# Performance work log

Hardware: AMD Instinct MI355X
Metric: run time of the kernel (lower is better)

Reference implementation:

```python
import jax, jax.numpy as jnp
import numpy as np

L, D, S, K, V, R, E, C = 256, 300, 16, 16, 100000, 6, 2048, 7
SW = 1            # slide_win; window = 2*SW+1 = 3
LAMB = 0.5
NEG = -1e9


def setup_inputs() -> dict:
    key = jax.random.key(0)
    ks = jax.random.split(key, 24)
    utt_emb = jax.random.normal(ks[0], (L, D), jnp.float32)
    str_src = jax.random.randint(ks[1], (E,), 0, L)
    str_dst = jax.random.randint(ks[2], (E,), 0, L)
    str_edge_type = jax.random.randint(ks[3], (E,), 0, R)
    src_ids = jax.random.randint(ks[4], (3, L, S), 0, V)
    src_valid = jax.random.uniform(ks[5], (3, L, S)) < 0.9
    cpt_src_ids = jnp.where(src_valid, src_ids, -1)
    dst_ids = jax.random.randint(ks[6], (3, L, S, K), 0, V)
    dst_valid = jnp.logical_and(jax.random.uniform(ks[7], (3, L, S, K)) < 0.8, src_valid[..., None])
    cpt_dst_ids = jnp.where(dst_valid, dst_ids, -1)
    cpt_weight = jax.random.uniform(ks[8], (3, L, S, K), jnp.float32)
    cpt_sentic = jax.random.normal(ks[9], (3, L, S, K), jnp.float32) * 0.5
    cpt_table = jax.random.normal(ks[10], (V, D), jnp.float32) * 0.02
    W_basis = jax.random.normal(ks[11], (2, D, D), jnp.float32) * 0.02
    comp = jax.random.normal(ks[12], (R, 2), jnp.float32)
    W_self = jax.random.normal(ks[13], (D, D), jnp.float32) * 0.02
    b_rgcn = jnp.zeros((D,), jnp.float32)
    Wq = jax.random.normal(ks[14], (D, D), jnp.float32) * 0.02
    Wk = jax.random.normal(ks[15], (D, D), jnp.float32) * 0.02
    Wv = jax.random.normal(ks[16], (D, D), jnp.float32) * 0.02
    Wo = jax.random.normal(ks[17], (D, D), jnp.float32) * 0.02
    r_vecs = jax.random.uniform(ks[18], (3, D), jnp.float32)  # isa/causes/hcontext relation vectors
    W_fuse = jax.random.normal(ks[19], (3 * D, D), jnp.float32) * 0.02
    b_fuse = jnp.zeros((D,), jnp.float32)
    W_out = jax.random.normal(ks[20], (D, C), jnp.float32) * 0.02
    b_out = jnp.zeros((C,), jnp.float32)
    return dict(utt_emb=utt_emb, str_src=str_src, str_dst=str_dst, str_edge_type=str_edge_type,
                cpt_src_ids=cpt_src_ids, cpt_dst_ids=cpt_dst_ids, cpt_weight=cpt_weight,
                cpt_sentic=cpt_sentic, cpt_table=cpt_table, W_basis=W_basis, comp=comp,
                W_self=W_self, b_rgcn=b_rgcn, Wq=Wq, Wk=Wk, Wv=Wv, Wo=Wo, r_vecs=r_vecs,
                W_fuse=W_fuse, b_fuse=b_fuse, W_out=W_out, b_out=b_out)


def reference(utt_emb, str_src, str_dst, str_edge_type, cpt_src_ids, cpt_dst_ids,
              cpt_weight, cpt_sentic, cpt_table, W_basis, comp, W_self, b_rgcn,
              Wq, Wk, Wv, Wo, r_vecs, W_fuse, b_fuse, W_out, b_out):
    H, dh, W = 2, D // 2, 2 * SW + 1
    # ---- RelGraphConv (basis decomposition, num_bases=2, sum aggregation + self-loop) ----
    W_rel = jnp.einsum('rb,bio->rio', comp, W_basis)                       # [R,D,D]
    msg = jnp.einsum('ei,eio->eo', utt_emb[str_src], W_rel[str_edge_type])  # [E,D]
    hidden_rgcn = jax.ops.segment_sum(msg, str_dst, num_segments=L) + utt_emb @ W_self + b_rgcn
    # ---- RelAtt: multi-head attention over sliding window, keep center utterance ----
    ids = jnp.concatenate([jnp.zeros((SW,), jnp.int32), jnp.arange(L, dtype=jnp.int32), jnp.full((SW,), L - 1, jnp.int32)])
    win = ids[jnp.arange(L)[:, None] + jnp.arange(W)[None, :]]             # [L,W]
    x = utt_emb[win]                                                       # [L,W,D]
    sh = lambda t: t.reshape(L, W, H, dh).transpose(0, 2, 1, 3)
    q, k, v = sh(x @ Wq), sh(x @ Wk), sh(x @ Wv)
    attn = jax.nn.softmax(jnp.einsum('lhqd,lhkd->lhqk', q, k) / jnp.sqrt(jnp.float32(dh)), axis=-1)
    relatt_out = (jnp.einsum('lhqk,lhkd->lhqd', attn, v).transpose(0, 2, 1, 3).reshape(L, W, D) @ Wo)[:, SW, :]
    # ---- symbolic reasoning over 3 relation types (padded, vectorized) ----
    src_mask = cpt_src_ids >= 0                                            # [3,L,S]
    dst_mask = cpt_dst_ids >= 0                                            # [3,L,S,K]
    src_emb = cpt_table[jnp.maximum(cpt_src_ids, 0)]                       # [3,L,S,D]
    dst_emb = cpt_table[jnp.maximum(cpt_dst_ids, 0)]                       # [3,L,S,K,D]
    u = relatt_out[None, :, None, None, :]                                 # [1,L,1,1,D]
    cos = jnp.abs(jnp.sum(u * dst_emb, -1) / (jnp.linalg.norm(relatt_out, axis=-1)[None, :, None, None] * jnp.linalg.norm(dst_emb, axis=-1) + 1e-8))
    omega = LAMB * cpt_weight * cos + (1.0 - LAMB) * jnp.abs(cpt_sentic)
    alpha1 = jax.nn.softmax(jnp.where(dst_mask, omega, NEG), axis=-1) * dst_mask  # [3,L,S,K]
    cpt = alpha1[..., None] * dst_emb                                      # [3,L,S,K,D]
    re_dot = r_vecs[:, None, None, None, :] * cpt                          # relation-weighted neighbor emb
    s = jnp.sum(src_emb[..., None, :] * re_dot, -1)                        # [3,L,S,K]
    alpha2 = jax.nn.softmax(jnp.where(dst_mask, s, NEG), axis=-1) * dst_mask
    src2 = src_emb + jnp.sum(alpha2[..., None] * re_dot, axis=3)           # [3,L,S,D]
    nodes = src2.transpose(1, 0, 2, 3).reshape(L, 3 * S, D)
    node_mask = src_mask.transpose(1, 0, 2).reshape(L, 3 * S)
    score = jnp.einsum('lnd,ld->ln', nodes, relatt_out)
    att = jax.nn.softmax(jnp.where(node_mask, score, NEG), axis=-1) * node_mask
    sym = jnp.einsum('ln,lnd->ld', att, nodes)
    sym = sym * jnp.any(node_mask, axis=-1, keepdims=True)                 # symbolic_mask
    # ---- fusion + classifier ----
    feat = jnp.concatenate([hidden_rgcn, relatt_out, sym], axis=-1)        # [L,3D]
    return jax.nn.log_softmax(jax.nn.relu(feat @ W_fuse + b_fuse) @ W_out + b_out, axis=-1)
```

## Files before the change

kernel.cpp:

```cpp
#include <hip/hip_runtime.h>
#include <math.h>

#define Lq 256
#define Dm 300
#define Sq 16
#define Kc 16
#define Eq 2048
#define D4 75

__global__ __launch_bounds__(256) void mm6_kernel(
    const float* __restrict__ utt,
    const float* __restrict__ Wb,
    const float* __restrict__ Wself,
    const float* __restrict__ brgcn,
    const float* __restrict__ Wq,
    const float* __restrict__ Wk,
    const float* __restrict__ Wv,
    float* __restrict__ P0, float* __restrict__ P1,
    float* __restrict__ Hrg, float* __restrict__ Q,
    float* __restrict__ Km, float* __restrict__ Vm)
{
    const int m = blockIdx.y;
    const float* W; float* Y; const float* bias = nullptr;
    switch (m) {
      case 0: W = Wb;          Y = P0; break;
      case 1: W = Wb + 90000;  Y = P1; break;
      case 2: W = Wself;       Y = Hrg; bias = brgcn; break;
      case 3: W = Wq;          Y = Q; break;
      case 4: W = Wk;          Y = Km; break;
      default: W = Wv;         Y = Vm; break;
    }
    const int row0 = blockIdx.x * 4;
    __shared__ float xs[4][Dm];
    for (int i = threadIdx.x; i < 4*Dm; i += 256)
        xs[i/Dm][i%Dm] = utt[(row0 + i/Dm)*Dm + (i%Dm)];
    __syncthreads();
    for (int c = threadIdx.x; c < Dm; c += 256) {
        float a0=0.f,a1=0.f,a2=0.f,a3=0.f;
        #pragma unroll 10
        for (int d = 0; d < Dm; ++d) {
            float wv = W[d*Dm + c];
            a0 += xs[0][d]*wv; a1 += xs[1][d]*wv;
            a2 += xs[2][d]*wv; a3 += xs[3][d]*wv;
        }
        float b = bias ? bias[c] : 0.f;
        Y[(row0+0)*Dm+c] = a0+b;
        Y[(row0+1)*Dm+c] = a1+b;
        Y[(row0+2)*Dm+c] = a2+b;
        Y[(row0+3)*Dm+c] = a3+b;
    }
}

__global__ __launch_bounds__(256) void mm4row_kernel(
    const float* __restrict__ X, const float* __restrict__ W, float* __restrict__ Y)
{
    const int row0 = blockIdx.x * 4;
    __shared__ float xs[4][Dm];
    for (int i = threadIdx.x; i < 4*Dm; i += 256)
        xs[i/Dm][i%Dm] = X[(row0 + i/Dm)*Dm + (i%Dm)];
    __syncthreads();
    for (int c = threadIdx.x; c < Dm; c += 256) {
        float a0=0.f,a1=0.f,a2=0.f,a3=0.f;
        #pragma unroll 10
        for (int d = 0; d < Dm; ++d) {
            float wv = W[d*Dm + c];
            a0 += xs[0][d]*wv; a1 += xs[1][d]*wv;
            a2 += xs[2][d]*wv; a3 += xs[3][d]*wv;
        }
        Y[(row0+0)*Dm+c] = a0;
        Y[(row0+1)*Dm+c] = a1;
        Y[(row0+2)*Dm+c] = a2;
        Y[(row0+3)*Dm+c] = a3;
    }
}

__global__ __launch_bounds__(64) void rgcn_edge_kernel(
    const int* __restrict__ src, const int* __restrict__ dst, const int* __restrict__ et,
    const float* __restrict__ comp, const float* __restrict__ P0,
    const float* __restrict__ P1, float* __restrict__ Hrg)
{
    int e = blockIdx.x;
    int s = src[e], d = dst[e], r = et[e];
    float c0 = comp[r*2], c1 = comp[r*2+1];
    for (int i = threadIdx.x; i < Dm; i += 64) {
        float msg = c0*P0[s*Dm+i] + c1*P1[s*Dm+i];
        atomicAdd(&Hrg[d*Dm+i], msg);
    }
}

__global__ __launch_bounds__(64) void winattn_kernel(
    const float* __restrict__ Q, const float* __restrict__ Kmat,
    const float* __restrict__ Vmat, float* __restrict__ ctx)
{
    int l = blockIdx.x;
    int lane = threadIdx.x;
    int w0 = l > 0 ? l-1 : 0;
    int w1 = l;
    int w2 = l < Lq-1 ? l+1 : Lq-1;
    int win[3] = {w0, w1, w2};
    __shared__ float sc[2][3];
    for (int h = 0; h < 2; ++h) {
      for (int w = 0; w < 3; ++w) {
        float acc = 0.f;
        const float* qp = Q + l*Dm + h*150;
        const float* kp = Kmat + win[w]*Dm + h*150;
        for (int d = lane; d < 150; d += 64) acc += qp[d]*kp[d];
        for (int off = 32; off > 0; off >>= 1) acc += __shfl_down(acc, off);
        if (lane == 0) sc[h][w] = acc * 0.081649658092772603f;
      }
    }
    __syncthreads();
    float attn[2][3];
    for (int h = 0; h < 2; ++h) {
      float m = fmaxf(sc[h][0], fmaxf(sc[h][1], sc[h][2]));
      float e0 = expf(sc[h][0]-m), e1 = expf(sc[h][1]-m), e2 = expf(sc[h][2]-m);
      float iz = 1.f/(e0+e1+e2);
      attn[h][0]=e0*iz; attn[h][1]=e1*iz; attn[h][2]=e2*iz;
    }
    for (int d = lane; d < Dm; d += 64) {
      int h = d / 150;
      ctx[l*Dm+d] = attn[h][0]*Vmat[w0*Dm+d] + attn[h][1]*Vmat[w1*Dm+d]
                  + attn[h][2]*Vmat[w2*Dm+d];
    }
}

__global__ __launch_bounds__(64) void rownorm_kernel(
    const float* __restrict__ X, float* __restrict__ nrm)
{
    int l = blockIdx.x;
    float acc = 0.f;
    for (int d = threadIdx.x; d < Dm; d += 64) { float v = X[l*Dm+d]; acc += v*v; }
    for (int off = 32; off > 0; off >>= 1) acc += __shfl_down(acc, off);
    if (threadIdx.x == 0) nrm[l] = sqrtf(acc);
}

__global__ __launch_bounds__(256) void concept_kernel(
    const int* __restrict__ src_ids,
    const int* __restrict__ dst_ids,
    const float* __restrict__ cw,
    const float* __restrict__ csen,
    const float* __restrict__ table,
    const float* __restrict__ relatt,
    const float* __restrict__ unorm,
    const float* __restrict__ rvecs,
    float* __restrict__ src2)
{
    int cell = blockIdx.x;
    int g = cell / (Lq*Sq);
    int l = (cell / Sq) % Lq;
    int tid = threadIdx.x, lane = tid & 63, wave = tid >> 6;

    __shared__ float4 s_rows[Kc][D4+1];
    __shared__ float4 s_u[D4+1], s_src[D4+1], s_r[D4+1], s_w[D4+1];
    __shared__ float  s_du[Kc], s_dw[Kc], s_dn[Kc], s_beta[Kc];
    __shared__ int    s_dst[Kc];

    const int base = cell * Kc;
    int sid = src_ids[cell];
    int srow = sid >= 0 ? sid : 0;
    if (tid < D4)              s_u[tid]        = ((const float4*)(relatt + l*Dm))[tid];
    else if (tid < 2*D4)       s_src[tid-D4]   = ((const float4*)(table + (size_t)srow*Dm))[tid-D4];
    else if (tid < 3*D4)       s_r[tid-2*D4]   = ((const float4*)(rvecs + g*Dm))[tid-2*D4];
    else if (tid < 3*D4+Kc)    s_dst[tid-3*D4] = dst_ids[base + tid - 3*D4];
    __syncthreads();
    if (tid < D4) {
        float4 a = s_src[tid], b = s_r[tid];
        s_w[tid] = make_float4(a.x*b.x, a.y*b.y, a.z*b.z, a.w*b.w);
    }
    __syncthreads();

    int grp = lane >> 4, gl = lane & 15;
    int k = wave*4 + grp;
    int did = s_dst[k];
    const float4* rp = (const float4*)(table + (size_t)(did >= 0 ? did : 0)*Dm);
    float du = 0.f, dw = 0.f, dn = 0.f;
    #pragma unroll
    for (int j = 0; j < 5; ++j) {
        int idx = gl + 16*j;
        if (idx < D4) {
            float4 v = rp[idx];
            s_rows[k][idx] = v;
            float4 u = s_u[idx], w = s_w[idx];
            du += v.x*u.x + v.y*u.y + v.z*u.z + v.w*u.w;
            dw += v.x*w.x + v.y*w.y + v.z*w.z + v.w*w.w;
            dn += v.x*v.x + v.y*v.y + v.z*v.z + v.w*v.w;
        }
    }
    #pragma unroll
    for (int off = 8; off; off >>= 1) {
        du += __shfl_down(du, off, 16);
        dw += __shfl_down(dw, off, 16);
        dn += __shfl_down(dn, off, 16);
    }
    if (gl == 0) { s_du[k] = du; s_dw[k] = dw; s_dn[k] = dn; }
    __syncthreads();

    if (wave == 0 && lane < Kc) {
        int kk = lane;
        int msk = (s_dst[kk] >= 0) ? 1 : 0;
        float pre = -1e30f;
        if (msk) {
            float cosv = fabsf(s_du[kk]) / (unorm[l]*sqrtf(s_dn[kk]) + 1e-8f);
            pre = 0.5f*cw[base+kk]*cosv + 0.5f*fabsf(csen[base+kk]);
        }
        float mx = pre;
        #pragma unroll
        for (int off = 8; off; off >>= 1) mx = fmaxf(mx, __shfl_xor(mx, off, 16));
        float e1 = msk ? expf(pre - mx) : 0.f;
        float Z = e1;
        #pragma unroll
        for (int off = 8; off; off >>= 1) Z += __shfl_xor(Z, off, 16);
        float beta = 0.f;
        if (Z > 0.f) {
            float a1 = e1 / Z;
            float sv = msk ? a1 * s_dw[kk] : -1e30f;
            float mx2 = sv;
            #pragma unroll
            for (int off = 8; off; off >>= 1) mx2 = fmaxf(mx2, __shfl_xor(mx2, off, 16));
            float e2 = msk ? expf(sv - mx2) : 0.f;
            float Z2 = e2;
            #pragma unroll
            for (int off = 8; off; off >>= 1) Z2 += __shfl_xor(Z2, off, 16);
            beta = a1 * (e2 / Z2);
        }
        s_beta[kk] = beta;
    }
    __syncthreads();

    if (tid < D4) {
        float4 acc = make_float4(0.f, 0.f, 0.f, 0.f);
        #pragma unroll
        for (int kk = 0; kk < Kc; ++kk) {
            float b = s_beta[kk];
            float4 v = s_rows[kk][tid];
            acc.x += b*v.x; acc.y += b*v.y; acc.z += b*v.z; acc.w += b*v.w;
        }
        float4 sv = s_src[tid], rv = s_r[tid];
        float4 o;
        o.x = sv.x + rv.x*acc.x;
        o.y = sv.y + rv.y*acc.y;
        o.z = sv.z + rv.z*acc.z;
        o.w = sv.w + rv.w*acc.w;
        ((float4*)(src2 + (size_t)cell*Dm))[tid] = o;
    }
}

__global__ __launch_bounds__(256) void sym_score_kernel(
    const int* __restrict__ src_ids, const float* __restrict__ src2,
    const float* __restrict__ relatt, float* __restrict__ score)
{
    int l = blockIdx.x, g = blockIdx.y;
    int tid = threadIdx.x, lane = tid & 63, wave = tid >> 6;
    __shared__ float4 s_u[D4+1];
    if (tid < D4) s_u[tid] = ((const float4*)(relatt + l*Dm))[tid];
    __syncthreads();
    int grp = lane >> 4, gl = lane & 15;
    int s = wave*4 + grp;
    const float4* rp = (const float4*)(src2 + (size_t)((g*Lq + l)*Sq + s)*Dm);
    float acc = 0.f;
    #pragma unroll
    for (int j = 0; j < 5; ++j) {
        int e = gl + 16*j;
        if (e < D4) {
            float4 v = rp[e], u = s_u[e];
            acc += v.x*u.x + v.y*u.y + v.z*u.z + v.w*u.w;
        }
    }
    #pragma unroll
    for (int off = 8; off; off >>= 1) acc += __shfl_down(acc, off, 16);
    if (gl == 0) {
        bool m = src_ids[(g*Lq + l)*Sq + s] >= 0;
        score[l*48 + g*Sq + s] = m ? acc : -1e30f;
    }
}

__global__ __launch_bounds__(128) void sym_apply_kernel(
    const float* __restrict__ score, const float* __restrict__ src2,
    float* __restrict__ sym)
{
    int l = blockIdx.x, tid = threadIdx.x;
    __shared__ float s_att[48];
    if (tid == 0) {
        float mx = -1e30f;
        for (int n = 0; n < 48; ++n) mx = fmaxf(mx, score[l*48+n]);
        float Z = 0.f;
        float e[48];
        for (int n = 0; n < 48; ++n) {
            float sv = score[l*48+n];
            e[n] = (sv > -1e29f) ? expf(sv-mx) : 0.f;
            Z += e[n];
        }
        float iZ = (Z > 0.f) ? 1.f/Z : 0.f;
        for (int n = 0; n < 48; ++n) s_att[n] = e[n]*iZ;
    }
    __syncthreads();
    if (tid < D4) {
        float4 acc = make_float4(0.f, 0.f, 0.f, 0.f);
        for (int n = 0; n < 48; ++n) {
            float a = s_att[n];
            if (a != 0.f) {
                int g = n >> 4, s = n & 15;
                float4 v = ((const float4*)(src2 + (size_t)((g*Lq + l)*Sq + s)*Dm))[tid];
                acc.x += a*v.x; acc.y += a*v.y; acc.z += a*v.z; acc.w += a*v.w;
            }
        }
        ((float4*)(sym + l*Dm))[tid] = acc;
    }
}

__global__ __launch_bounds__(256) void fuse1_kernel(
    const float* __restrict__ Hrg, const float* __restrict__ relatt,
    const float* __restrict__ sym, const float* __restrict__ Wf,
    float* __restrict__ part)
{
    int l = blockIdx.x, j = blockIdx.y, tid = threadIdx.x;
    const int k0 = j * 100;
    const int seg = j / 3;
    const int koff = (j % 3) * 100;
    const float* srcp = (seg == 0) ? Hrg : (seg == 1) ? relatt : sym;
    __shared__ float s_f[100];
    if (tid < 100) s_f[tid] = srcp[l*Dm + koff + tid];
    __syncthreads();
    for (int c = tid; c < Dm; c += 256) {
        float acc = 0.f;
        #pragma unroll 10
        for (int i = 0; i < 100; ++i)
            acc += s_f[i] * Wf[(k0 + i)*Dm + c];
        part[(size_t)j*Lq*Dm + l*Dm + c] = acc;
    }
}

__global__ __launch_bounds__(256) void fuse2_kernel(
    const float* __restrict__ part, const float* __restrict__ bf,
    const float* __restrict__ Wout, const float* __restrict__ bout,
    float* __restrict__ out)
{
    int l = blockIdx.x, tid = threadIdx.x;
    __shared__ float s_h1[Dm];
    __shared__ float s_logit[7];
    for (int c = tid; c < Dm; c += 256) {
        float acc = bf[c];
        #pragma unroll
        for (int j = 0; j < 9; ++j)
            acc += part[(size_t)j*Lq*Dm + l*Dm + c];
        s_h1[c] = fmaxf(acc, 0.f);
    }
    __syncthreads();
    if (tid < 64) {
        for (int c = 0; c < 7; ++c) {
            float acc = 0.f;
            for (int i = tid; i < Dm; i += 64) acc += s_h1[i]*Wout[i*7+c];
            for (int off = 32; off > 0; off >>= 1) acc += __shfl_down(acc, off);
            if (tid == 0) s_logit[c] = acc + bout[c];
        }
    }
    __syncthreads();
    if (tid == 0) {
        float mx = s_logit[0];
        for (int c = 1; c < 7; ++c) mx = fmaxf(mx, s_logit[c]);
        float Z = 0.f;
        for (int c = 0; c < 7; ++c) Z += expf(s_logit[c]-mx);
        float lz = logf(Z) + mx;
        for (int c = 0; c < 7; ++c) out[l*7+c] = s_logit[c] - lz;
    }
}

extern "C" void kernel_launch(void* const* d_in, const int* in_sizes, int n_in,
                              void* d_out, int out_size, void* d_ws, size_t ws_size,
                              hipStream_t stream)
{
    const float* utt   = (const float*)d_in[0];
    const int* str_src = (const int*)d_in[1];
    const int* str_dst = (const int*)d_in[2];
    const int* str_et  = (const int*)d_in[3];
    const int* csrc    = (const int*)d_in[4];
    const int* cdst    = (const int*)d_in[5];
    const float* cw    = (const float*)d_in[6];
    const float* csen  = (const float*)d_in[7];
    const float* table = (const float*)d_in[8];
    const float* Wb    = (const float*)d_in[9];
    const float* comp  = (const float*)d_in[10];
    const float* Wself = (const float*)d_in[11];
    const float* brg   = (const float*)d_in[12];
    const float* Wq    = (const float*)d_in[13];
    const float* Wk    = (const float*)d_in[14];
    const float* Wv    = (const float*)d_in[15];
    const float* Wo    = (const float*)d_in[16];
    const float* rvec  = (const float*)d_in[17];
    const float* Wf    = (const float*)d_in[18];
    const float* bf    = (const float*)d_in[19];
    const float* Wout  = (const float*)d_in[20];
    const float* bout  = (const float*)d_in[21];

    float* ws   = (float*)d_ws;
    float* P0   = ws;
    float* P1   = P0 + 76800;
    float* Q    = P1 + 76800;
    float* Km   = Q  + 76800;
    float* Vm   = Km + 76800;
    float* Hrg  = Vm + 76800;
    float* ctx  = Hrg + 76800;
    float* rel  = ctx + 76800;
    float* sym  = rel + 76800;
    float* unrm = sym + 76800;
    float* score= unrm + 256;
    float* part = score + 12288;
    float* src2 = part + 691200;

    mm6_kernel<<<dim3(64,6), 256, 0, stream>>>(utt, Wb, Wself, brg, Wq, Wk, Wv,
                                               P0, P1, Hrg, Q, Km, Vm);
    rgcn_edge_kernel<<<Eq, 64, 0, stream>>>(str_src, str_dst, str_et, comp, P0, P1, Hrg);
    winattn_kernel<<<Lq, 64, 0, stream>>>(Q, Km, Vm, ctx);
    mm4row_kernel<<<64, 256, 0, stream>>>(ctx, Wo, rel);
    rownorm_kernel<<<Lq, 64, 0, stream>>>(rel, unrm);
    concept_kernel<<<3*Lq*Sq, 256, 0, stream>>>(csrc, cdst, cw, csen, table, rel,
                                                unrm, rvec, src2);
    sym_score_kernel<<<dim3(Lq,3), 256, 0, stream>>>(csrc, src2, rel, score);
    sym_apply_kernel<<<Lq, 128, 0, stream>>>(score, src2, sym);
    fuse1_kernel<<<dim3(Lq,9), 256, 0, stream>>>(Hrg, rel, sym, Wf, part);
    fuse2_kernel<<<Lq, 256, 0, stream>>>(part, bf, Wout, bout, (float*)d_out);
}
```

Measured before the change: 375.6 us.

## Fuse row norm into Wo matmul and symbolic score into concept kernel

Folds the row-norm computation into the output-projection matmul epilogue, which removes the rownorm launch. It also computes the symbolic attention score inside the concept kernel, so sym_score_kernel and its re-read of src2 go away. The concept kernel stops staging the 16 neighbor rows in shared memory and instead re-reads them from global memory (likely cache hits) only when the weight is nonzero. This lowers LDS use and may raise occupancy, at the cost of a second global gather per neighbor.

New measurement: 394.6 us. 5.0% more time.

```diff
diff --git a/kernel.cpp b/kernel.cpp
--- a/kernel.cpp
+++ b/kernel.cpp
@@ -51,15 +51,20 @@
     }
 }
 
-__global__ __launch_bounds__(256) void mm4row_kernel(
-    const float* __restrict__ X, const float* __restrict__ W, float* __restrict__ Y)
+__global__ __launch_bounds__(256) void mm4row_norm_kernel(
+    const float* __restrict__ X, const float* __restrict__ W,
+    float* __restrict__ Y, float* __restrict__ nrm)
 {
     const int row0 = blockIdx.x * 4;
+    const int tid = threadIdx.x, lane = tid & 63;
     __shared__ float xs[4][Dm];
-    for (int i = threadIdx.x; i < 4*Dm; i += 256)
+    __shared__ float s_n[4];
+    for (int i = tid; i < 4*Dm; i += 256)
         xs[i/Dm][i%Dm] = X[(row0 + i/Dm)*Dm + (i%Dm)];
-    __syncthreads();
-    for (int c = threadIdx.x; c < Dm; c += 256) {
+    if (tid < 4) s_n[tid] = 0.f;
+    __syncthreads();
+    float sq0=0.f, sq1=0.f, sq2=0.f, sq3=0.f;
+    for (int c = tid; c < Dm; c += 256) {
         float a0=0.f,a1=0.f,a2=0.f,a3=0.f;
         #pragma unroll 10
         for (int d = 0; d < Dm; ++d) {
@@ -71,7 +76,21 @@
         Y[(row0+1)*Dm+c] = a1;
         Y[(row0+2)*Dm+c] = a2;
         Y[(row0+3)*Dm+c] = a3;
-    }
+        sq0 += a0*a0; sq1 += a1*a1; sq2 += a2*a2; sq3 += a3*a3;
+    }
+    #pragma unroll
+    for (int off = 32; off; off >>= 1) {
+        sq0 += __shfl_down(sq0, off);
+        sq1 += __shfl_down(sq1, off);
+        sq2 += __shfl_down(sq2, off);
+        sq3 += __shfl_down(sq3, off);
+    }
+    if (lane == 0) {
+        atomicAdd(&s_n[0], sq0); atomicAdd(&s_n[1], sq1);
+        atomicAdd(&s_n[2], sq2); atomicAdd(&s_n[3], sq3);
+    }
+    __syncthreads();
+    if (tid < 4) nrm[row0 + tid] = sqrtf(s_n[tid]);
 }
 
 __global__ __launch_bounds__(64) void rgcn_edge_kernel(
@@ -124,16 +143,6 @@
     }
 }
 
-__global__ __launch_bounds__(64) void rownorm_kernel(
-    const float* __restrict__ X, float* __restrict__ nrm)
-{
-    int l = blockIdx.x;
-    float acc = 0.f;
-    for (int d = threadIdx.x; d < Dm; d += 64) { float v = X[l*Dm+d]; acc += v*v; }
-    for (int off = 32; off > 0; off >>= 1) acc += __shfl_down(acc, off);
-    if (threadIdx.x == 0) nrm[l] = sqrtf(acc);
-}
-
 __global__ __launch_bounds__(256) void concept_kernel(
     const int* __restrict__ src_ids,
     const int* __restrict__ dst_ids,
@@ -143,16 +152,18 @@
     const float* __restrict__ relatt,
     const float* __restrict__ unorm,
     const float* __restrict__ rvecs,
-    float* __restrict__ src2)
+    float* __restrict__ src2,
+    float* __restrict__ score)
 {
     int cell = blockIdx.x;
     int g = cell / (Lq*Sq);
     int l = (cell / Sq) % Lq;
+    int s = cell % Sq;
     int tid = threadIdx.x, lane = tid & 63, wave = tid >> 6;
 
-    __shared__ float4 s_rows[Kc][D4+1];
     __shared__ float4 s_u[D4+1], s_src[D4+1], s_r[D4+1], s_w[D4+1];
     __shared__ float  s_du[Kc], s_dw[Kc], s_dn[Kc], s_beta[Kc];
+    __shared__ float  s_part[16];
     __shared__ int    s_dst[Kc];
 
     const int base = cell * Kc;
@@ -179,7 +190,6 @@
         int idx = gl + 16*j;
         if (idx < D4) {
             float4 v = rp[idx];
-            s_rows[k][idx] = v;
             float4 u = s_u[idx], w = s_w[idx];
             du += v.x*u.x + v.y*u.y + v.z*u.z + v.w*u.w;
             dw += v.x*w.x + v.y*w.y + v.z*w.z + v.w*w.w;
@@ -227,13 +237,16 @@
     }
     __syncthreads();
 
+    float dot = 0.f;
     if (tid < D4) {
         float4 acc = make_float4(0.f, 0.f, 0.f, 0.f);
         #pragma unroll
         for (int kk = 0; kk < Kc; ++kk) {
             float b = s_beta[kk];
-            float4 v = s_rows[kk][tid];
-            acc.x += b*v.x; acc.y += b*v.y; acc.z += b*v.z; acc.w += b*v.w;
+            if (b != 0.f) {
+                float4 v = ((const float4*)(table + (size_t)s_dst[kk]*Dm))[tid];
+                acc.x += b*v.x; acc.y += b*v.y; acc.z += b*v.z; acc.w += b*v.w;
+            }
         }
         float4 sv = s_src[tid], rv = s_r[tid];
         float4 o;
@@ -242,35 +255,17 @@
         o.z = sv.z + rv.z*acc.z;
         o.w = sv.w + rv.w*acc.w;
         ((float4*)(src2 + (size_t)cell*Dm))[tid] = o;
-    }
-}
-
-__global__ __launch_bounds__(256) void sym_score_kernel(
-    const int* __restrict__ src_ids, const float* __restrict__ src2,
-    const float* __restrict__ relatt, float* __restrict__ score)
-{
-    int l = blockIdx.x, g = blockIdx.y;
-    int tid = threadIdx.x, lane = tid & 63, wave = tid >> 6;
-    __shared__ float4 s_u[D4+1];
-    if (tid < D4) s_u[tid] = ((const float4*)(relatt + l*Dm))[tid];
-    __syncthreads();
-    int grp = lane >> 4, gl = lane & 15;
-    int s = wave*4 + grp;
-    const float4* rp = (const float4*)(src2 + (size_t)((g*Lq + l)*Sq + s)*Dm);
-    float acc = 0.f;
-    #pragma unroll
-    for (int j = 0; j < 5; ++j) {
-        int e = gl + 16*j;
-        if (e < D4) {
-            float4 v = rp[e], u = s_u[e];
-            acc += v.x*u.x + v.y*u.y + v.z*u.z + v.w*u.w;
-        }
-    }
-    #pragma unroll
-    for (int off = 8; off; off >>= 1) acc += __shfl_down(acc, off, 16);
-    if (gl == 0) {
-        bool m = src_ids[(g*Lq + l)*Sq + s] >= 0;
-        score[l*48 + g*Sq + s] = m ? acc : -1e30f;
+        float4 u = s_u[tid];
+        dot = o.x*u.x + o.y*u.y + o.z*u.z + o.w*u.w;
+    }
+    if (wave == 1 && lane < 16) s_part[lane] = dot;
+    __syncthreads();
+    if (wave == 0) {
+        float v = dot + (lane < 16 ? s_part[lane] : 0.f);
+        #pragma unroll
+        for (int off = 32; off; off >>= 1) v += __shfl_down(v, off);
+        if (lane == 0)
+            score[l*48 + g*Sq + s] = (sid >= 0) ? v : -1e30f;
     }
 }
 
@@ -411,11 +406,9 @@
                                                P0, P1, Hrg, Q, Km, Vm);
     rgcn_edge_kernel<<<Eq, 64, 0, stream>>>(str_src, str_dst, str_et, comp, P0, P1, Hrg);
     winattn_kernel<<<Lq, 64, 0, stream>>>(Q, Km, Vm, ctx);
-    mm4row_kernel<<<64, 256, 0, stream>>>(ctx, Wo, rel);
-    rownorm_kernel<<<Lq, 64, 0, stream>>>(rel, unrm);
+    mm4row_norm_kernel<<<64, 256, 0, stream>>>(ctx, Wo, rel, unrm);
     concept_kernel<<<3*Lq*Sq, 256, 0, stream>>>(csrc, cdst, cw, csen, table, rel,
-                                                unrm, rvec, src2);
-    sym_score_kernel<<<dim3(Lq,3), 256, 0, stream>>>(csrc, src2, rel, score);
+                                                unrm, rvec, src2, score);
     sym_apply_kernel<<<Lq, 128, 0, stream>>>(score, src2, sym);
     fuse1_kernel<<<dim3(Lq,9), 256, 0, stream>>>(Hrg, rel, sym, Wf, part);
     fuse2_kernel<<<Lq, 256, 0, stream>>>(part, bf, Wout, bout, (float*)d_out);
```
